# Kernel tuning notes

Measured on AMD Instinct MI355X. Metric: run time of the kernel, lower is better.

## Reference

```python
import jax, jax.numpy as jnp
import numpy as np
import math

D_INNER = 512
D_STATE = 16
DT_RANK = 32
B_SZ = 2
L_SEQ = 4096


def setup_inputs() -> dict:
    key = jax.random.key(0)
    ks = jax.random.split(key, 6)
    x = jax.random.normal(ks[0], (B_SZ, L_SEQ, D_INNER), dtype=jnp.float32)
    # parameters (match torch init semantics closely enough for a numeric baseline)
    A = jnp.arange(1, D_STATE + 1, dtype=jnp.float32)
    A_log = jnp.broadcast_to(jnp.log(A)[None, :], (D_INNER, D_STATE)).copy()
    D_param = jnp.ones((D_INNER,), dtype=jnp.float32)
    # x_proj: Linear(d_inner -> dt_rank + 2*d_state), no bias
    W_xproj = jax.random.normal(ks[1], (DT_RANK + 2 * D_STATE, D_INNER), dtype=jnp.float32) / np.sqrt(D_INNER)
    # dt_proj: Linear(dt_rank -> d_inner) with special bias init
    W_dt = jax.random.normal(ks[2], (D_INNER, DT_RANK), dtype=jnp.float32) / np.sqrt(DT_RANK)
    dt_init = jnp.exp(jax.random.uniform(ks[3], (D_INNER,)) * (math.log(0.1) - math.log(0.001)) + math.log(0.001))
    b_dt = jnp.log(jnp.exp(dt_init) - 1.0)
    alpha = jnp.asarray(0.6, dtype=jnp.float32)
    beta_logit = jnp.asarray(math.log(0.99 / (1.0 - 0.99 + 1e-08)), dtype=jnp.float32)
    return {"x": x, "A_log": A_log, "D_param": D_param, "W_xproj": W_xproj,
            "W_dt": W_dt, "b_dt": b_dt, "alpha": alpha, "beta_logit": beta_logit}


def _momentum_ssm(x, A_log, D_param, W_xproj, W_dt, b_dt, alpha, beta_logit):
    # x: (B, L, D)
    proj = jnp.einsum('bld,pd->blp', x, W_xproj)            # (B, L, r+2N)
    dt_in = proj[..., :DT_RANK]
    Bp = proj[..., DT_RANK:DT_RANK + D_STATE]                # (B, L, N)
    Cp = proj[..., DT_RANK + D_STATE:]                       # (B, L, N)
    dt = jax.nn.softplus(jnp.einsum('blr,dr->bld', dt_in, W_dt) + b_dt)  # (B, L, D)
    A = -jnp.exp(A_log)                                      # (D, N)
    A_bar = jnp.exp(dt[..., None] * A[None, None])           # (B, L, D, N)
    # fused B_bar * x_t: dt * Bp * x
    inp = dt[..., None] * Bp[:, :, None, :] * x[..., None]   # (B, L, D, N)
    beta = jax.nn.sigmoid(beta_logit)

    # scan over time; carry (h, v): (B, D, N)
    h0 = jnp.zeros((x.shape[0], D_INNER, D_STATE), dtype=x.dtype)
    v0 = jnp.zeros_like(h0)

    def step(carry, ts):
        h, v = carry
        a_t, inp_t, c_t = ts                                 # (B,D,N), (B,D,N), (B,N)
        v = beta * v + alpha * inp_t
        h = a_t * h + v
        y = jnp.einsum('bdn,bn->bd', h, c_t)
        return (h, v), y

    xs = (jnp.moveaxis(A_bar, 1, 0), jnp.moveaxis(inp, 1, 0), jnp.moveaxis(Cp, 1, 0))
    _, ys = jax.lax.scan(step, (h0, v0), xs)                 # ys: (L, B, D)
    y = jnp.moveaxis(ys, 0, 1)                               # (B, L, D)
    return y + D_param * x


def reference(x, A_log, D_param, W_xproj, W_dt, b_dt, alpha, beta_logit):
    return _momentum_ssm(x, A_log, D_param, W_xproj, W_dt, b_dt, alpha, beta_logit)
```

## Files before the change

kernel.cpp:

```cpp
#include <hip/hip_runtime.h>


#define D_IN 512
#define D_ST 16
#define DTR  32
#define BSZ  2
#define LSEQ 4096
#define PDIM 64
#define NCH  256
#define LCH  (LSEQ / NCH)
#define LOG2E 1.44269504f
#define LN2   0.69314718f

typedef __attribute__((ext_vector_type(8))) short short8;
typedef __attribute__((ext_vector_type(4))) float f32x4;
typedef _Float16 f16;
typedef __attribute__((ext_vector_type(8))) _Float16 f16x8;

__device__ inline float fast_exp2(float x) { return __builtin_amdgcn_exp2f(x); }
__device__ inline float fast_log2(float x) { return __builtin_amdgcn_logf(x); }

__device__ inline unsigned short bf16_rne(float f) {
  unsigned b = __float_as_uint(f);
  return (unsigned short)((b + 0x7fffu + ((b >> 16) & 1u)) >> 16);
}

__device__ inline void cvt8(const float4 u, const float4 v, short8& hi, short8& lo) {
  float f[8] = {u.x, u.y, u.z, u.w, v.x, v.y, v.z, v.w};
#pragma unroll
  for (int i = 0; i < 8; ++i) {
    unsigned short h = bf16_rne(f[i]);
    hi[i] = (short)h;
    float r = f[i] - __uint_as_float((unsigned)h << 16);
    lo[i] = (short)bf16_rne(r);
  }
}

__device__ inline void st16h(f16* p, const float* s) {
  f16 t[16];
#pragma unroll
  for (int i = 0; i < 16; ++i) t[i] = (f16)s[i];
  *(f16x8*)p = *(f16x8*)&t[0];
  *(f16x8*)(p + 8) = *(f16x8*)&t[8];
}
__device__ inline void ld16h(const f16* p, float* d) {
  f16x8 a = *(const f16x8*)p;
  f16x8 b = *(const f16x8*)(p + 8);
#pragma unroll
  for (int i = 0; i < 8; ++i) { d[i] = (float)a[i]; d[8 + i] = (float)b[i]; }
}

__device__ inline bool loadA2(const float* A_log, int d, float* A2) {
  const float4* ap = (const float4*)(A_log + (size_t)d * D_ST);
#pragma unroll
  for (int i = 0; i < 4; ++i) {
    float4 a4 = ap[i];
    A2[4 * i + 0] = -__expf(a4.x) * LOG2E;
    A2[4 * i + 1] = -__expf(a4.y) * LOG2E;
    A2[4 * i + 2] = -__expf(a4.z) * LOG2E;
    A2[4 * i + 3] = -__expf(a4.w) * LOG2E;
  }
  bool pw = true;
#pragma unroll
  for (int n = 1; n < 16; ++n) {
    float ref = (float)(n + 1) * A2[0];
    pw = pw && (fabsf(A2[n] - ref) <= 2e-5f * fabsf(ref));
  }
  return pw;
}

__global__ __launch_bounds__(256) void k_wprep(const float* __restrict__ W,
                                               short* __restrict__ Whi,
                                               short* __restrict__ Wlo) {
  const int i = (blockIdx.x * 256 + threadIdx.x) * 4;
  float4 w = *(const float4*)(W + i);
  float f[4] = {w.x, w.y, w.z, w.w};
  unsigned short h[4], lo[4];
#pragma unroll
  for (int j = 0; j < 4; ++j) {
    h[j] = bf16_rne(f[j]);
    float r = f[j] - __uint_as_float((unsigned)h[j] << 16);
    lo[j] = bf16_rne(r);
  }
  *(uint2*)(Whi + i) = make_uint2(h[0] | ((unsigned)h[1] << 16), h[2] | ((unsigned)h[3] << 16));
  *(uint2*)(Wlo + i) = make_uint2(lo[0] | ((unsigned)lo[1] << 16), lo[2] | ((unsigned)lo[3] << 16));
}

#define MM3(ACC, AH, AL, BH, BL)                                        \
  ACC = __builtin_amdgcn_mfma_f32_16x16x32_bf16(AL, BH, ACC, 0, 0, 0);  \
  ACC = __builtin_amdgcn_mfma_f32_16x16x32_bf16(AH, BL, ACC, 0, 0, 0);  \
  ACC = __builtin_amdgcn_mfma_f32_16x16x32_bf16(AH, BH, ACC, 0, 0, 0);

#define LOADB(P, S)                                   \
  {                                                   \
    const int kb = ((S) & 15) * 32;                   \
    P##h0 = *(const short8*)(bh + kb);                \
    P##h1 = *(const short8*)(bh + 8192 + kb);         \
    P##h2 = *(const short8*)(bh + 16384 + kb);        \
    P##h3 = *(const short8*)(bh + 24576 + kb);        \
    P##l0 = *(const short8*)(bl + kb);                \
    P##l1 = *(const short8*)(bl + 8192 + kb);         \
    P##l2 = *(const short8*)(bl + 16384 + kb);        \
    P##l3 = *(const short8*)(bl + 24576 + kb);        \
  }

#define LOADA(Aa, Ab, S)                              \
  {                                                   \
    const int ka = ((S) & 15) * 32;                   \
    Aa = *(const float4*)(xr + ka);                   \
    Ab = *(const float4*)(xr + ka + 4);               \
  }

#define SUBSTEP(Aa, Ab, P, SA, SB)                    \
  {                                                   \
    short8 ahi, alo;                                  \
    cvt8(Aa, Ab, ahi, alo);                           \
    MM3(acc0, ahi, alo, P##h0, P##l0);                \
    MM3(acc1, ahi, alo, P##h1, P##l1);                \
    MM3(acc2, ahi, alo, P##h2, P##l2);                \
    MM3(acc3, ahi, alo, P##h3, P##l3);                \
    LOADB(P, SB);                                     \
    LOADA(Aa, Ab, SA);                                \
  }

__global__ __launch_bounds__(64) void k_proj(const float* __restrict__ x,
                                             const short* __restrict__ Whi,
                                             const short* __restrict__ Wlo,
                                             float* __restrict__ proj) {
  const int row0 = blockIdx.x * 16;
  const int l = threadIdx.x;
  const int m = l & 15;
  const int ko = (l >> 4) * 8;
  const float* xr = x + (size_t)(row0 + m) * D_IN + ko;
  const short* bh = Whi + (size_t)m * D_IN + ko;
  const short* bl = Wlo + (size_t)m * D_IN + ko;

  f32x4 acc0 = {0.f, 0.f, 0.f, 0.f}, acc1 = acc0, acc2 = acc0, acc3 = acc0;
  float4 A0a, A0b, A1a, A1b, A2a, A2b, A3a, A3b;
  short8 Xh0, Xh1, Xh2, Xh3, Xl0, Xl1, Xl2, Xl3;
  short8 Yh0, Yh1, Yh2, Yh3, Yl0, Yl1, Yl2, Yl3;
  LOADA(A0a, A0b, 0); LOADA(A1a, A1b, 1); LOADA(A2a, A2b, 2); LOADA(A3a, A3b, 3);
  LOADB(X, 0); LOADB(Y, 1);

#pragma unroll
  for (int it = 0; it < 4; ++it) {
    const int s = it * 4;
    SUBSTEP(A0a, A0b, X, s + 4, s + 2);
    SUBSTEP(A1a, A1b, Y, s + 5, s + 3);
    SUBSTEP(A2a, A2b, X, s + 6, s + 4);
    SUBSTEP(A3a, A3b, Y, s + 7, s + 5);
  }

  const int r0 = (l >> 4) * 4;
#pragma unroll
  for (int r = 0; r < 4; ++r) {
    float* pr = proj + (size_t)(row0 + r0 + r) * PDIM + m;
    pr[0] = acc0[r]; pr[16] = acc1[r]; pr[32] = acc2[r]; pr[48] = acc3[r];
  }
}

#define S1_BODY(GET_A)                                        \
  _Pragma("unroll")                                           \
  for (int j = 0; j < LCH; ++j) {                             \
    const float dtc = dtv[j], xv = xs[j];                     \
    sd += dtc;                                                \
    bpow *= beta;                                             \
    const float u = alpha * dtc * xv;                         \
    GET_A;                                                    \
    float4 Bq[4];                                             \
    _Pragma("unroll")                                         \
    for (int i = 0; i < 4; ++i) Bq[i] = ((const float4*)&Ps[j][DTR])[i]; \
    const float* Bf = (const float*)Bq;                       \
    float ar = 1.f;                                           \
    _Pragma("unroll")                                         \
    for (int n = 0; n < 16; ++n) {                            \
      NEXT_A(ar, n);                                          \
      v[n] = fmaf(beta, v[n], u * Bf[n]);                     \
      h[n] = fmaf(ar, h[n], v[n]);                            \
      cv[n] = fmaf(ar, cv[n], bpow);                          \
    }                                                         \
  }

__global__ __launch_bounds__(256) void k_scan1(const float* __restrict__ x,
                                               const float* __restrict__ proj,
                                               const float* __restrict__ A_log,
                                               const float* __restrict__ W_dt,
                                               const float* __restrict__ b_dt,
                                               const float* __restrict__ alpha_p,
                                               const float* __restrict__ beta_p,
                                               f16* __restrict__ hh,
                                               f16* __restrict__ vh,
                                               f16* __restrict__ cvv,
                                               float* __restrict__ sdt,
                                               f16* __restrict__ dth) {
  __shared__ float Ps[LCH][PDIM];
  const int c = blockIdx.x, b = blockIdx.z;
  const int d = blockIdx.y * 256 + threadIdx.x;
  const int t0 = c * LCH;
  {
    const float4* src = (const float4*)(proj + ((size_t)b * LSEQ + t0) * PDIM);
    ((float4*)&Ps[0][0])[threadIdx.x] = src[threadIdx.x];
  }
  float xs[LCH];
  {
    const float* xp = x + ((size_t)b * LSEQ + t0) * D_IN + d;
#pragma unroll
    for (int j = 0; j < LCH; ++j) xs[j] = xp[(size_t)j * D_IN];
  }
  const float alpha = alpha_p[0];
  const float beta = 1.f / (1.f + __expf(-beta_p[0]));
  float A2[D_ST];
  const bool powA = loadA2(A_log, d, A2);
  __syncthreads();

  float dtv[LCH];
  {
    float4 w4[8];
    const float4* wp = (const float4*)(W_dt + (size_t)d * DTR);
#pragma unroll
    for (int i = 0; i < 8; ++i) w4[i] = wp[i];
    const float bb = b_dt[d];
#pragma unroll
    for (int j = 0; j < LCH; ++j) {
      const float4* pj = (const float4*)&Ps[j][0];
      float a0 = bb, a1 = 0.f, a2 = 0.f, a3 = 0.f;
#pragma unroll
      for (int k = 0; k < 8; ++k) {
        float4 p = pj[k];
        a0 = fmaf(p.x, w4[k].x, a0);
        a1 = fmaf(p.y, w4[k].y, a1);
        a2 = fmaf(p.z, w4[k].z, a2);
        a3 = fmaf(p.w, w4[k].w, a3);
      }
      float acc = (a0 + a1) + (a2 + a3);
      float e = fast_exp2(acc * LOG2E);
      dtv[j] = (acc > 20.f) ? acc : LN2 * fast_log2(1.f + e);
    }
  }
  {
    f16* dp = dth + ((size_t)b * LSEQ + t0) * D_IN + d;
#pragma unroll
    for (int j = 0; j < LCH; ++j) dp[(size_t)j * D_IN] = (f16)dtv[j];
  }

  float h[16] = {}, v[16] = {}, cv[16] = {};
  float bpow = 1.f, sd = 0.f;
  if (powA) {
#define NEXT_A(ar, n) ar *= r
    S1_BODY(const float r = fast_exp2(dtc * A2[0]))
#undef NEXT_A
  } else {
#define NEXT_A(ar, n) ar = fast_exp2(dtc * A2[n])
    S1_BODY()
#undef NEXT_A
  }

  const size_t base = ((size_t)(b * NCH + c) * D_IN + d) * D_ST;
  st16h(hh + base, h);
  st16h(vh + base, v);
  st16h(cvv + base, cv);
  sdt[(size_t)(b * NCH + c) * D_IN + d] = sd;
}

__global__ __launch_bounds__(64) void k_fix(f16* __restrict__ hh,
                                            f16* __restrict__ vh,
                                            const f16* __restrict__ cvv,
                                            const float* __restrict__ sdt,
                                            const float* __restrict__ A_log,
                                            const float* __restrict__ beta_p) {
  const int g = blockIdx.x * 64 + threadIdx.x;
  const int b = g >> 13;
  const int dn = g & 8191;
  const float beta = 1.f / (1.f + __expf(-beta_p[0]));
  const float A2 = -__expf(A_log[dn]) * LOG2E;
  float bL = beta;
#pragma unroll
  for (int i = 0; i < 4; ++i) bL *= bL;

  const size_t cs = (size_t)D_IN * D_ST;
  const size_t base = (size_t)b * NCH * cs + dn;
  const size_t sbase = (size_t)b * NCH * D_IN + (dn >> 4);

  float hg[8], vg[8], cg[8], sg[8];
#pragma unroll
  for (int i = 0; i < 8; ++i) {
    hg[i] = (float)hh[base + i * cs];
    vg[i] = (float)vh[base + i * cs];
    cg[i] = (float)cvv[base + i * cs];
    sg[i] = sdt[sbase + i * D_IN];
  }
  float H = 0.f, V = 0.f;
  for (int c0 = 0; c0 < NCH; c0 += 8) {
    const int cp = (c0 + 8) & (NCH - 1);
    float hn[8], vn[8], cn[8], sn[8];
#pragma unroll
    for (int i = 0; i < 8; ++i) {
      hn[i] = (float)hh[base + (size_t)(cp + i) * cs];
      vn[i] = (float)vh[base + (size_t)(cp + i) * cs];
      cn[i] = (float)cvv[base + (size_t)(cp + i) * cs];
      sn[i] = sdt[sbase + (size_t)(cp + i) * D_IN];
    }
#pragma unroll
    for (int i = 0; i < 8; ++i) {
      hh[base + (size_t)(c0 + i) * cs] = (f16)H;
      vh[base + (size_t)(c0 + i) * cs] = (f16)V;
      const float Pa = fast_exp2(sg[i] * A2);
      const float Hn = fmaf(Pa, H, fmaf(cg[i], V, hg[i]));
      V = fmaf(bL, V, vg[i]);
      H = Hn;
    }
#pragma unroll
    for (int i = 0; i < 8; ++i) { hg[i] = hn[i]; vg[i] = vn[i]; cg[i] = cn[i]; sg[i] = sn[i]; }
  }
}

#define S2_BODY(GET_A)                                        \
  _Pragma("unroll")                                           \
  for (int j = 0; j < LCH; ++j) {                             \
    const float dtc = dtv[j], xv = xs[j];                     \
    const float u = alpha * dtc * xv;                         \
    GET_A;                                                    \
    float4 Bq[8];                                             \
    _Pragma("unroll")                                         \
    for (int i = 0; i < 8; ++i) Bq[i] = ((const float4*)&Ps[j][DTR])[i]; \
    const float* Bf = (const float*)Bq;                       \
    float y0 = 0.f, y1 = 0.f, y2 = 0.f, y3 = 0.f;             \
    float ar = 1.f;                                           \
    _Pragma("unroll")                                         \
    for (int n = 0; n < 16; ++n) {                            \
      NEXT_A(ar, n);                                          \
      v[n] = fmaf(beta, v[n], u * Bf[n]);                     \
      h[n] = fmaf(ar, h[n], v[n]);                            \
      float hc = h[n] * Bf[16 + n];                           \
      if ((n & 3) == 0) y0 += hc;                             \
      else if ((n & 3) == 1) y1 += hc;                        \
      else if ((n & 3) == 2) y2 += hc;                        \
      else y3 += hc;                                          \
    }                                                         \
    op[(size_t)j * D_IN] = (y0 + y1) + (y2 + y3) + Dv * xv;   \
  }

__global__ __launch_bounds__(256) void k_scan2(const float* __restrict__ x,
                                               const f16* __restrict__ dth,
                                               const float* __restrict__ proj,
                                               const float* __restrict__ A_log,
                                               const float* __restrict__ D_param,
                                               const float* __restrict__ alpha_p,
                                               const float* __restrict__ beta_p,
                                               const f16* __restrict__ hh,
                                               const f16* __restrict__ vh,
                                               float* __restrict__ out) {
  __shared__ float Ps[LCH][PDIM];
  const int c = blockIdx.x, b = blockIdx.z;
  const int d = blockIdx.y * 256 + threadIdx.x;
  const int t0 = c * LCH;
  {
    const float4* src = (const float4*)(proj + ((size_t)b * LSEQ + t0) * PDIM);
    ((float4*)&Ps[0][0])[threadIdx.x] = src[threadIdx.x];
  }
  float xs[LCH], dtv[LCH];
  {
    const float* xp = x + ((size_t)b * LSEQ + t0) * D_IN + d;
    const f16* dp = dth + ((size_t)b * LSEQ + t0) * D_IN + d;
#pragma unroll
    for (int j = 0; j < LCH; ++j) xs[j] = xp[(size_t)j * D_IN];
#pragma unroll
    for (int j = 0; j < LCH; ++j) dtv[j] = (float)dp[(size_t)j * D_IN];
  }
  const float alpha = alpha_p[0];
  const float beta = 1.f / (1.f + __expf(-beta_p[0]));
  const float Dv = D_param[d];
  float A2[D_ST];
  const bool powA = loadA2(A_log, d, A2);
  const size_t ibase = ((size_t)(b * NCH + c) * D_IN + d) * D_ST;
  float h[16], v[16];
  ld16h(hh + ibase, h);
  ld16h(vh + ibase, v);
  __syncthreads();

  float* op = out + ((size_t)b * LSEQ + t0) * D_IN + d;
  if (powA) {
#define NEXT_A(ar, n) ar *= r
    S2_BODY(const float r = fast_exp2(dtc * A2[0]))
#undef NEXT_A
  } else {
#define NEXT_A(ar, n) ar = fast_exp2(dtc * A2[n])
    S2_BODY()
#undef NEXT_A
  }
}

extern "C" void kernel_launch(void* const* d_in, const int* in_sizes, int n_in,
                              void* d_out, int out_size, void* d_ws, size_t ws_size,
                              hipStream_t stream) {
  const float* x = (const float*)d_in[0];
  const float* A_log = (const float*)d_in[1];
  const float* D_param = (const float*)d_in[2];
  const float* W_xproj = (const float*)d_in[3];
  const float* W_dt = (const float*)d_in[4];
  const float* b_dt = (const float*)d_in[5];
  const float* alpha = (const float*)d_in[6];
  const float* beta_logit = (const float*)d_in[7];
  float* out = (float*)d_out;

  const size_t NST = (size_t)BSZ * NCH * D_IN * D_ST;
  float* ws = (float*)d_ws;
  float* proj = ws;
  float* sdt = proj + (size_t)BSZ * LSEQ * PDIM;
  f16* hh = (f16*)(sdt + (size_t)BSZ * NCH * D_IN);
  f16* vh = hh + NST;
  f16* cvv = vh + NST;
  f16* dth = cvv + NST;
  short* Whi = (short*)(dth + (size_t)BSZ * LSEQ * D_IN);
  short* Wlo = Whi + (size_t)PDIM * D_IN;

  k_wprep<<<dim3(PDIM * D_IN / 1024), dim3(256), 0, stream>>>(W_xproj, Whi, Wlo);
  k_proj<<<dim3(BSZ * LSEQ / 16), dim3(64), 0, stream>>>(x, Whi, Wlo, proj);
  k_scan1<<<dim3(NCH, D_IN / 256, BSZ), dim3(256), 0, stream>>>(
      x, proj, A_log, W_dt, b_dt, alpha, beta_logit, hh, vh, cvv, sdt, dth);
  k_fix<<<dim3(BSZ * D_IN * D_ST / 64), dim3(64), 0, stream>>>(hh, vh, cvv, sdt, A_log,
                                                               beta_logit);
  k_scan2<<<dim3(NCH, D_IN / 256, BSZ), dim3(256), 0, stream>>>(
      x, dth, proj, A_log, D_param, alpha, beta_logit, hh, vh, out);
}
```

Before: 171.9 us.

## Fuse all stages into one persistent kernel with grid-wide atomic barriers

Merges weight prep, projection, chunk scan, chunk-state fixup and the output scan into a single 512-block kernel, separating the phases with software grid barriers built on an atomic counter. Chunk count drops from 256 to 128, so each block handles 32 timesteps and the fixup serial chain is halved. dt is now kept in registers between the chunk scan and the output scan instead of being written to and reread from global memory in fp16. This removes four kernel launch gaps and the dt round trip. In exchange it relies on all 512 blocks being co-resident, adds an extra memset, and idles most blocks during the projection and fixup phases.

```diff
diff --git a/kernel.cpp b/kernel.cpp
--- a/kernel.cpp
+++ b/kernel.cpp
@@ -7,8 +7,9 @@
 #define BSZ  2
 #define LSEQ 4096
 #define PDIM 64
-#define NCH  256
+#define NCH  128
 #define LCH  (LSEQ / NCH)
+#define NBLK 512
 #define LOG2E 1.44269504f
 #define LN2   0.69314718f
 
@@ -69,21 +70,17 @@
   return pw;
 }
 
-__global__ __launch_bounds__(256) void k_wprep(const float* __restrict__ W,
-                                               short* __restrict__ Whi,
-                                               short* __restrict__ Wlo) {
-  const int i = (blockIdx.x * 256 + threadIdx.x) * 4;
-  float4 w = *(const float4*)(W + i);
-  float f[4] = {w.x, w.y, w.z, w.w};
-  unsigned short h[4], lo[4];
-#pragma unroll
-  for (int j = 0; j < 4; ++j) {
-    h[j] = bf16_rne(f[j]);
-    float r = f[j] - __uint_as_float((unsigned)h[j] << 16);
-    lo[j] = bf16_rne(r);
-  }
-  *(uint2*)(Whi + i) = make_uint2(h[0] | ((unsigned)h[1] << 16), h[2] | ((unsigned)h[3] << 16));
-  *(uint2*)(Wlo + i) = make_uint2(lo[0] | ((unsigned)lo[1] << 16), lo[2] | ((unsigned)lo[3] << 16));
+__device__ inline void gbar(unsigned* cnt, unsigned target) {
+  __syncthreads();
+  if (threadIdx.x == 0) {
+    __threadfence();
+    __hip_atomic_fetch_add(cnt, 1u, __ATOMIC_RELEASE, __HIP_MEMORY_SCOPE_AGENT);
+    while (__hip_atomic_load(cnt, __ATOMIC_ACQUIRE, __HIP_MEMORY_SCOPE_AGENT) < target) {
+      __builtin_amdgcn_s_sleep(2);
+    }
+    __threadfence();
+  }
+  __syncthreads();
 }
 
 #define MM3(ACC, AH, AL, BH, BL)                                        \
@@ -123,43 +120,7 @@
     LOADA(Aa, Ab, SA);                                \
   }
 
-__global__ __launch_bounds__(64) void k_proj(const float* __restrict__ x,
-                                             const short* __restrict__ Whi,
-                                             const short* __restrict__ Wlo,
-                                             float* __restrict__ proj) {
-  const int row0 = blockIdx.x * 16;
-  const int l = threadIdx.x;
-  const int m = l & 15;
-  const int ko = (l >> 4) * 8;
-  const float* xr = x + (size_t)(row0 + m) * D_IN + ko;
-  const short* bh = Whi + (size_t)m * D_IN + ko;
-  const short* bl = Wlo + (size_t)m * D_IN + ko;
-
-  f32x4 acc0 = {0.f, 0.f, 0.f, 0.f}, acc1 = acc0, acc2 = acc0, acc3 = acc0;
-  float4 A0a, A0b, A1a, A1b, A2a, A2b, A3a, A3b;
-  short8 Xh0, Xh1, Xh2, Xh3, Xl0, Xl1, Xl2, Xl3;
-  short8 Yh0, Yh1, Yh2, Yh3, Yl0, Yl1, Yl2, Yl3;
-  LOADA(A0a, A0b, 0); LOADA(A1a, A1b, 1); LOADA(A2a, A2b, 2); LOADA(A3a, A3b, 3);
-  LOADB(X, 0); LOADB(Y, 1);
-
-#pragma unroll
-  for (int it = 0; it < 4; ++it) {
-    const int s = it * 4;
-    SUBSTEP(A0a, A0b, X, s + 4, s + 2);
-    SUBSTEP(A1a, A1b, Y, s + 5, s + 3);
-    SUBSTEP(A2a, A2b, X, s + 6, s + 4);
-    SUBSTEP(A3a, A3b, Y, s + 7, s + 5);
-  }
-
-  const int r0 = (l >> 4) * 4;
-#pragma unroll
-  for (int r = 0; r < 4; ++r) {
-    float* pr = proj + (size_t)(row0 + r0 + r) * PDIM + m;
-    pr[0] = acc0[r]; pr[16] = acc1[r]; pr[32] = acc2[r]; pr[48] = acc3[r];
-  }
-}
-
-#define S1_BODY(GET_A)                                        \
+#define P2_BODY(GET_A)                                        \
   _Pragma("unroll")                                           \
   for (int j = 0; j < LCH; ++j) {                             \
     const float dtc = dtv[j], xv = xs[j];                     \
@@ -181,140 +142,7 @@
     }                                                         \
   }
 
-__global__ __launch_bounds__(256) void k_scan1(const float* __restrict__ x,
-                                               const float* __restrict__ proj,
-                                               const float* __restrict__ A_log,
-                                               const float* __restrict__ W_dt,
-                                               const float* __restrict__ b_dt,
-                                               const float* __restrict__ alpha_p,
-                                               const float* __restrict__ beta_p,
-                                               f16* __restrict__ hh,
-                                               f16* __restrict__ vh,
-                                               f16* __restrict__ cvv,
-                                               float* __restrict__ sdt,
-                                               f16* __restrict__ dth) {
-  __shared__ float Ps[LCH][PDIM];
-  const int c = blockIdx.x, b = blockIdx.z;
-  const int d = blockIdx.y * 256 + threadIdx.x;
-  const int t0 = c * LCH;
-  {
-    const float4* src = (const float4*)(proj + ((size_t)b * LSEQ + t0) * PDIM);
-    ((float4*)&Ps[0][0])[threadIdx.x] = src[threadIdx.x];
-  }
-  float xs[LCH];
-  {
-    const float* xp = x + ((size_t)b * LSEQ + t0) * D_IN + d;
-#pragma unroll
-    for (int j = 0; j < LCH; ++j) xs[j] = xp[(size_t)j * D_IN];
-  }
-  const float alpha = alpha_p[0];
-  const float beta = 1.f / (1.f + __expf(-beta_p[0]));
-  float A2[D_ST];
-  const bool powA = loadA2(A_log, d, A2);
-  __syncthreads();
-
-  float dtv[LCH];
-  {
-    float4 w4[8];
-    const float4* wp = (const float4*)(W_dt + (size_t)d * DTR);
-#pragma unroll
-    for (int i = 0; i < 8; ++i) w4[i] = wp[i];
-    const float bb = b_dt[d];
-#pragma unroll
-    for (int j = 0; j < LCH; ++j) {
-      const float4* pj = (const float4*)&Ps[j][0];
-      float a0 = bb, a1 = 0.f, a2 = 0.f, a3 = 0.f;
-#pragma unroll
-      for (int k = 0; k < 8; ++k) {
-        float4 p = pj[k];
-        a0 = fmaf(p.x, w4[k].x, a0);
-        a1 = fmaf(p.y, w4[k].y, a1);
-        a2 = fmaf(p.z, w4[k].z, a2);
-        a3 = fmaf(p.w, w4[k].w, a3);
-      }
-      float acc = (a0 + a1) + (a2 + a3);
-      float e = fast_exp2(acc * LOG2E);
-      dtv[j] = (acc > 20.f) ? acc : LN2 * fast_log2(1.f + e);
-    }
-  }
-  {
-    f16* dp = dth + ((size_t)b * LSEQ + t0) * D_IN + d;
-#pragma unroll
-    for (int j = 0; j < LCH; ++j) dp[(size_t)j * D_IN] = (f16)dtv[j];
-  }
-
-  float h[16] = {}, v[16] = {}, cv[16] = {};
-  float bpow = 1.f, sd = 0.f;
-  if (powA) {
-#define NEXT_A(ar, n) ar *= r
-    S1_BODY(const float r = fast_exp2(dtc * A2[0]))
-#undef NEXT_A
-  } else {
-#define NEXT_A(ar, n) ar = fast_exp2(dtc * A2[n])
-    S1_BODY()
-#undef NEXT_A
-  }
-
-  const size_t base = ((size_t)(b * NCH + c) * D_IN + d) * D_ST;
-  st16h(hh + base, h);
-  st16h(vh + base, v);
-  st16h(cvv + base, cv);
-  sdt[(size_t)(b * NCH + c) * D_IN + d] = sd;
-}
-
-__global__ __launch_bounds__(64) void k_fix(f16* __restrict__ hh,
-                                            f16* __restrict__ vh,
-                                            const f16* __restrict__ cvv,
-                                            const float* __restrict__ sdt,
-                                            const float* __restrict__ A_log,
-                                            const float* __restrict__ beta_p) {
-  const int g = blockIdx.x * 64 + threadIdx.x;
-  const int b = g >> 13;
-  const int dn = g & 8191;
-  const float beta = 1.f / (1.f + __expf(-beta_p[0]));
-  const float A2 = -__expf(A_log[dn]) * LOG2E;
-  float bL = beta;
-#pragma unroll
-  for (int i = 0; i < 4; ++i) bL *= bL;
-
-  const size_t cs = (size_t)D_IN * D_ST;
-  const size_t base = (size_t)b * NCH * cs + dn;
-  const size_t sbase = (size_t)b * NCH * D_IN + (dn >> 4);
-
-  float hg[8], vg[8], cg[8], sg[8];
-#pragma unroll
-  for (int i = 0; i < 8; ++i) {
-    hg[i] = (float)hh[base + i * cs];
-    vg[i] = (float)vh[base + i * cs];
-    cg[i] = (float)cvv[base + i * cs];
-    sg[i] = sdt[sbase + i * D_IN];
-  }
-  float H = 0.f, V = 0.f;
-  for (int c0 = 0; c0 < NCH; c0 += 8) {
-    const int cp = (c0 + 8) & (NCH - 1);
-    float hn[8], vn[8], cn[8], sn[8];
-#pragma unroll
-    for (int i = 0; i < 8; ++i) {
-      hn[i] = (float)hh[base + (size_t)(cp + i) * cs];
-      vn[i] = (float)vh[base + (size_t)(cp + i) * cs];
-      cn[i] = (float)cvv[base + (size_t)(cp + i) * cs];
-      sn[i] = sdt[sbase + (size_t)(cp + i) * D_IN];
-    }
-#pragma unroll
-    for (int i = 0; i < 8; ++i) {
-      hh[base + (size_t)(c0 + i) * cs] = (f16)H;
-      vh[base + (size_t)(c0 + i) * cs] = (f16)V;
-      const float Pa = fast_exp2(sg[i] * A2);
-      const float Hn = fmaf(Pa, H, fmaf(cg[i], V, hg[i]));
-      V = fmaf(bL, V, vg[i]);
-      H = Hn;
-    }
-#pragma unroll
-    for (int i = 0; i < 8; ++i) { hg[i] = hn[i]; vg[i] = vn[i]; cg[i] = cn[i]; sg[i] = sn[i]; }
-  }
-}
-
-#define S2_BODY(GET_A)                                        \
+#define P4_BODY(GET_A)                                        \
   _Pragma("unroll")                                           \
   for (int j = 0; j < LCH; ++j) {                             \
     const float dtc = dtv[j], xv = xs[j];                     \
@@ -340,53 +168,197 @@
     op[(size_t)j * D_IN] = (y0 + y1) + (y2 + y3) + Dv * xv;   \
   }
 
-__global__ __launch_bounds__(256) void k_scan2(const float* __restrict__ x,
-                                               const f16* __restrict__ dth,
-                                               const float* __restrict__ proj,
-                                               const float* __restrict__ A_log,
-                                               const float* __restrict__ D_param,
-                                               const float* __restrict__ alpha_p,
-                                               const float* __restrict__ beta_p,
-                                               const f16* __restrict__ hh,
-                                               const f16* __restrict__ vh,
-                                               float* __restrict__ out) {
+__global__ __launch_bounds__(256, 2) void k_fused(
+    const float* __restrict__ x, const float* __restrict__ A_log,
+    const float* __restrict__ D_param, const float* __restrict__ W_xproj,
+    const float* __restrict__ W_dt, const float* __restrict__ b_dt,
+    const float* __restrict__ alpha_p, const float* __restrict__ beta_p,
+    float* __restrict__ out, unsigned* __restrict__ bar, float* __restrict__ proj,
+    float* __restrict__ sdt, f16* __restrict__ hh, f16* __restrict__ vh,
+    f16* __restrict__ cvv, short* __restrict__ Whi, short* __restrict__ Wlo) {
+  const int tid = threadIdx.x;
+  const int bx = blockIdx.x;
   __shared__ float Ps[LCH][PDIM];
-  const int c = blockIdx.x, b = blockIdx.z;
-  const int d = blockIdx.y * 256 + threadIdx.x;
-  const int t0 = c * LCH;
-  {
-    const float4* src = (const float4*)(proj + ((size_t)b * LSEQ + t0) * PDIM);
-    ((float4*)&Ps[0][0])[threadIdx.x] = src[threadIdx.x];
-  }
-  float xs[LCH], dtv[LCH];
-  {
-    const float* xp = x + ((size_t)b * LSEQ + t0) * D_IN + d;
-    const f16* dp = dth + ((size_t)b * LSEQ + t0) * D_IN + d;
-#pragma unroll
-    for (int j = 0; j < LCH; ++j) xs[j] = xp[(size_t)j * D_IN];
-#pragma unroll
-    for (int j = 0; j < LCH; ++j) dtv[j] = (float)dp[(size_t)j * D_IN];
-  }
+
+  if (bx < 32) {
+    const int i = (bx * 256 + tid) * 4;
+    float4 w = *(const float4*)(W_xproj + i);
+    float f[4] = {w.x, w.y, w.z, w.w};
+    unsigned short h4[4], l4[4];
+#pragma unroll
+    for (int j = 0; j < 4; ++j) {
+      h4[j] = bf16_rne(f[j]);
+      float r = f[j] - __uint_as_float((unsigned)h4[j] << 16);
+      l4[j] = bf16_rne(r);
+    }
+    *(uint2*)(Whi + i) =
+        make_uint2(h4[0] | ((unsigned)h4[1] << 16), h4[2] | ((unsigned)h4[3] << 16));
+    *(uint2*)(Wlo + i) =
+        make_uint2(l4[0] | ((unsigned)l4[1] << 16), l4[2] | ((unsigned)l4[3] << 16));
+  }
+  gbar(bar, 1 * NBLK);
+
+  if (tid < 64) {
+    const int row0 = bx * 16;
+    const int m = tid & 15;
+    const int ko = (tid >> 4) * 8;
+    const float* xr = x + (size_t)(row0 + m) * D_IN + ko;
+    const short* bh = Whi + (size_t)m * D_IN + ko;
+    const short* bl = Wlo + (size_t)m * D_IN + ko;
+
+    f32x4 acc0 = {0.f, 0.f, 0.f, 0.f}, acc1 = acc0, acc2 = acc0, acc3 = acc0;
+    float4 A0a, A0b, A1a, A1b, A2a, A2b, A3a, A3b;
+    short8 Xh0, Xh1, Xh2, Xh3, Xl0, Xl1, Xl2, Xl3;
+    short8 Yh0, Yh1, Yh2, Yh3, Yl0, Yl1, Yl2, Yl3;
+    LOADA(A0a, A0b, 0); LOADA(A1a, A1b, 1); LOADA(A2a, A2b, 2); LOADA(A3a, A3b, 3);
+    LOADB(X, 0); LOADB(Y, 1);
+#pragma unroll
+    for (int it = 0; it < 4; ++it) {
+      const int s = it * 4;
+      SUBSTEP(A0a, A0b, X, s + 4, s + 2);
+      SUBSTEP(A1a, A1b, Y, s + 5, s + 3);
+      SUBSTEP(A2a, A2b, X, s + 6, s + 4);
+      SUBSTEP(A3a, A3b, Y, s + 7, s + 5);
+    }
+    const int r0 = (tid >> 4) * 4;
+#pragma unroll
+    for (int r = 0; r < 4; ++r) {
+      float* pr = proj + (size_t)(row0 + r0 + r) * PDIM + m;
+      pr[0] = acc0[r]; pr[16] = acc1[r]; pr[32] = acc2[r]; pr[48] = acc3[r];
+    }
+  }
+  gbar(bar, 2 * NBLK);
+
   const float alpha = alpha_p[0];
   const float beta = 1.f / (1.f + __expf(-beta_p[0]));
-  const float Dv = D_param[d];
+  const int c = bx & (NCH - 1);
+  const int b = bx >> 8;
+  const int d = ((bx >> 7) & 1) * 256 + tid;
+  const int t0 = c * LCH;
+  const size_t base = ((size_t)(b * NCH + c) * D_IN + d) * D_ST;
+
+  {
+    const float4* src = (const float4*)(proj + ((size_t)b * LSEQ + t0) * PDIM);
+    float4* dst = (float4*)&Ps[0][0];
+    dst[tid] = src[tid];
+    dst[tid + 256] = src[tid + 256];
+  }
+  float xs[LCH];
+  {
+    const float* xp = x + ((size_t)b * LSEQ + t0) * D_IN + d;
+#pragma unroll
+    for (int j = 0; j < LCH; ++j) xs[j] = xp[(size_t)j * D_IN];
+  }
   float A2[D_ST];
   const bool powA = loadA2(A_log, d, A2);
-  const size_t ibase = ((size_t)(b * NCH + c) * D_IN + d) * D_ST;
-  float h[16], v[16];
-  ld16h(hh + ibase, h);
-  ld16h(vh + ibase, v);
   __syncthreads();
 
-  float* op = out + ((size_t)b * LSEQ + t0) * D_IN + d;
-  if (powA) {
+  float dtv[LCH];
+  {
+    float4 w4[8];
+    const float4* wp = (const float4*)(W_dt + (size_t)d * DTR);
+#pragma unroll
+    for (int i = 0; i < 8; ++i) w4[i] = wp[i];
+    const float bb = b_dt[d];
+#pragma unroll
+    for (int j = 0; j < LCH; ++j) {
+      const float4* pj = (const float4*)&Ps[j][0];
+      float a0 = bb, a1 = 0.f, a2 = 0.f, a3 = 0.f;
+#pragma unroll
+      for (int k = 0; k < 8; ++k) {
+        float4 p = pj[k];
+        a0 = fmaf(p.x, w4[k].x, a0);
+        a1 = fmaf(p.y, w4[k].y, a1);
+        a2 = fmaf(p.z, w4[k].z, a2);
+        a3 = fmaf(p.w, w4[k].w, a3);
+      }
+      float acc = (a0 + a1) + (a2 + a3);
+      float e = fast_exp2(acc * LOG2E);
+      dtv[j] = (acc > 20.f) ? acc : LN2 * fast_log2(1.f + e);
+    }
+  }
+
+  {
+    float h[16] = {}, v[16] = {}, cv[16] = {};
+    float bpow = 1.f, sd = 0.f;
+    if (powA) {
 #define NEXT_A(ar, n) ar *= r
-    S2_BODY(const float r = fast_exp2(dtc * A2[0]))
+      P2_BODY(const float r = fast_exp2(dtc * A2[0]))
 #undef NEXT_A
-  } else {
+    } else {
 #define NEXT_A(ar, n) ar = fast_exp2(dtc * A2[n])
-    S2_BODY()
+      P2_BODY()
 #undef NEXT_A
+    }
+    st16h(hh + base, h);
+    st16h(vh + base, v);
+    st16h(cvv + base, cv);
+    sdt[(size_t)(b * NCH + c) * D_IN + d] = sd;
+  }
+  gbar(bar, 3 * NBLK);
+
+  if (bx < 64) {
+    const int g = bx * 256 + tid;
+    const int b3 = g >> 13;
+    const int dn = g & 8191;
+    const float A2f = -__expf(A_log[dn]) * LOG2E;
+    float bL = beta;
+#pragma unroll
+    for (int i = 0; i < 5; ++i) bL *= bL;
+
+    const size_t cs = (size_t)D_IN * D_ST;
+    const size_t fb = (size_t)b3 * NCH * cs + dn;
+    const size_t sb = (size_t)b3 * NCH * D_IN + (dn >> 4);
+
+    float hg[8], vg[8], cg[8], sg[8];
+#pragma unroll
+    for (int i = 0; i < 8; ++i) {
+      hg[i] = (float)hh[fb + i * cs];
+      vg[i] = (float)vh[fb + i * cs];
+      cg[i] = (float)cvv[fb + i * cs];
+      sg[i] = sdt[sb + i * D_IN];
+    }
+    float H = 0.f, V = 0.f;
+    for (int c0 = 0; c0 < NCH; c0 += 8) {
+      const int cp = (c0 + 8) & (NCH - 1);
+      float hn[8], vn[8], cn[8], sn[8];
+#pragma unroll
+      for (int i = 0; i < 8; ++i) {
+        hn[i] = (float)hh[fb + (size_t)(cp + i) * cs];
+        vn[i] = (float)vh[fb + (size_t)(cp + i) * cs];
+        cn[i] = (float)cvv[fb + (size_t)(cp + i) * cs];
+        sn[i] = sdt[sb + (size_t)(cp + i) * D_IN];
+      }
+#pragma unroll
+      for (int i = 0; i < 8; ++i) {
+        hh[fb + (size_t)(c0 + i) * cs] = (f16)H;
+        vh[fb + (size_t)(c0 + i) * cs] = (f16)V;
+        const float Pa = fast_exp2(sg[i] * A2f);
+        const float Hn = fmaf(Pa, H, fmaf(cg[i], V, hg[i]));
+        V = fmaf(bL, V, vg[i]);
+        H = Hn;
+      }
+#pragma unroll
+      for (int i = 0; i < 8; ++i) { hg[i] = hn[i]; vg[i] = vn[i]; cg[i] = cn[i]; sg[i] = sn[i]; }
+    }
+  }
+  gbar(bar, 4 * NBLK);
+
+  {
+    const float Dv = D_param[d];
+    float h[16], v[16];
+    ld16h(hh + base, h);
+    ld16h(vh + base, v);
+    float* op = out + ((size_t)b * LSEQ + t0) * D_IN + d;
+    if (powA) {
+#define NEXT_A(ar, n) ar *= r
+      P4_BODY(const float r = fast_exp2(dtc * A2[0]))
+#undef NEXT_A
+    } else {
+#define NEXT_A(ar, n) ar = fast_exp2(dtc * A2[n])
+      P4_BODY()
+#undef NEXT_A
+    }
   }
 }
 
@@ -404,22 +376,17 @@
   float* out = (float*)d_out;
 
   const size_t NST = (size_t)BSZ * NCH * D_IN * D_ST;
-  float* ws = (float*)d_ws;
-  float* proj = ws;
+  unsigned* bar = (unsigned*)d_ws;
+  float* proj = (float*)((char*)d_ws + 256);
   float* sdt = proj + (size_t)BSZ * LSEQ * PDIM;
   f16* hh = (f16*)(sdt + (size_t)BSZ * NCH * D_IN);
   f16* vh = hh + NST;
   f16* cvv = vh + NST;
-  f16* dth = cvv + NST;
-  short* Whi = (short*)(dth + (size_t)BSZ * LSEQ * D_IN);
+  short* Whi = (short*)(cvv + NST);
   short* Wlo = Whi + (size_t)PDIM * D_IN;
 
-  k_wprep<<<dim3(PDIM * D_IN / 1024), dim3(256), 0, stream>>>(W_xproj, Whi, Wlo);
-  k_proj<<<dim3(BSZ * LSEQ / 16), dim3(64), 0, stream>>>(x, Whi, Wlo, proj);
-  k_scan1<<<dim3(NCH, D_IN / 256, BSZ), dim3(256), 0, stream>>>(
-      x, proj, A_log, W_dt, b_dt, alpha, beta_logit, hh, vh, cvv, sdt, dth);
-  k_fix<<<dim3(BSZ * D_IN * D_ST / 64), dim3(64), 0, stream>>>(hh, vh, cvv, sdt, A_log,
-                                                               beta_logit);
-  k_scan2<<<dim3(NCH, D_IN / 256, BSZ), dim3(256), 0, stream>>>(
-      x, dth, proj, A_log, D_param, alpha, beta_logit, hh, vh, out);
-}
+  hipMemsetAsync(d_ws, 0, 256, stream);
+  k_fused<<<dim3(NBLK), dim3(256), 0, stream>>>(x, A_log, D_param, W_xproj, W_dt, b_dt,
+                                                alpha, beta_logit, out, bar, proj, sdt,
+                                                hh, vh, cvv, Whi, Wlo);
+}
```

Result: slower. 454.7 us (+164.6%).
